# Kernel tuning notes

Hardware: AMD Instinct MI355X
Metric: run time of the kernel (lower is better)

The kernel has to match this reference:

```python
import jax, jax.numpy as jnp
import numpy as np

B, L, H = 16, 2048, 768
V, D = 30000, 64


def setup_inputs() -> dict:
    key = jax.random.key(0)
    k1, k2, k3, k4 = jax.random.split(key, 4)
    bert_x = jax.random.normal(k1, (B, L, H), dtype=jnp.float32)
    x = jax.random.randint(k2, (B, L), 0, V, dtype=jnp.int64)
    ae = jax.random.normal(k3, (V, D), dtype=jnp.float32)
    w = jax.random.normal(k4, (D, D), dtype=jnp.float32)
    return {"bert_x": bert_x, "x": x, "ae": ae, "w": w}


def reference(bert_x, x, ae, w):
    # E[b,i] = ae[x[b,i]]  -> [B, L, D]
    E = ae[x]
    # fac[b,i,j] = E[b,i] @ w @ E[b,j]   (bilinear pairwise score)
    scores = jnp.einsum('bid,de,bje->bij', E, w, E)
    Lseq = bert_x.shape[1]
    i = jnp.arange(Lseq, dtype=bert_x.dtype)[:, None]
    j = jnp.arange(Lseq, dtype=bert_x.dtype)[None, :]
    # strictly-causal weight (i+1)/(j+1) for i < j, zero elsewhere
    coef = jnp.where(i < j, (i + 1.0) / (j + 1.0), 0.0).astype(bert_x.dtype)
    # res[:, j] = bert_x[:, j] + sum_{i<j} bert_x[:, i] * coef[i,j] * fac[b,i,j]
    res = bert_x + jnp.einsum('bij,bih->bjh', scores * coef, bert_x)
    return res
```

## Files before the change

kernel.cpp:

```cpp
#include <hip/hip_runtime.h>

#define Bb 16
#define Ll 2048
#define Hh 768
#define Dd 64
#define Cc 64
#define HC 48
#define NT (Hh / HC)
#define NCH (Ll / Cc)

typedef __attribute__((ext_vector_type(8))) short bf16x8;
typedef __attribute__((ext_vector_type(4))) float f32x4;

__device__ __forceinline__ short f2bf(float f) {
  union { float f; unsigned u; } c;
  c.f = f;
  unsigned r = (c.u + 0x7FFFu + ((c.u >> 16) & 1u)) >> 16;
  return (short)r;
}
__device__ __forceinline__ unsigned pack2(float a, float b) {
  return (unsigned)(unsigned short)f2bf(a) | ((unsigned)(unsigned short)f2bf(b) << 16);
}

__global__ __launch_bounds__(256) void prep_kernel(const int* __restrict__ x,
                                                   const float* __restrict__ ae,
                                                   const float* __restrict__ w,
                                                   short* __restrict__ Eg,
                                                   short* __restrict__ FTg,
                                                   short* __restrict__ scTg) {
  const int b = blockIdx.x >> 5;
  const int ch = blockIdx.x & 31;
  const int tid = threadIdx.x;
  __shared__ float sE[64 * 68];
  __shared__ float sW[64 * 68];
  __shared__ float sF[64 * 68];
  const size_t gb = (size_t)blockIdx.x * 4096;

  {
    const int i = tid >> 2, seg = tid & 3;
    const int idx = x[b * Ll + ch * Cc + i];
    const float4* aer = (const float4*)(ae + (size_t)idx * Dd);
    float4 ev[4];
#pragma unroll
    for (int q = 0; q < 4; ++q) {
      ev[q] = aer[seg * 4 + q];
      *(float4*)&sE[i * 68 + seg * 16 + q * 4] = ev[q];
    }
    uint4 p0v, p1v;
    p0v.x = pack2(ev[0].x, ev[0].y); p0v.y = pack2(ev[0].z, ev[0].w);
    p0v.z = pack2(ev[1].x, ev[1].y); p0v.w = pack2(ev[1].z, ev[1].w);
    p1v.x = pack2(ev[2].x, ev[2].y); p1v.y = pack2(ev[2].z, ev[2].w);
    p1v.z = pack2(ev[3].x, ev[3].y); p1v.w = pack2(ev[3].z, ev[3].w);
    *(uint4*)(Eg + gb + i * 64 + seg * 16) = p0v;
    *(uint4*)(Eg + gb + i * 64 + seg * 16 + 8) = p1v;
    const float4* wr = (const float4*)w;
#pragma unroll
    for (int q = 0; q < 4; ++q) {
      const int fl = q * 256 + tid;
      const int r = fl >> 4, cc = fl & 15;
      *(float4*)&sW[r * 68 + cc * 4] = wr[fl];
    }
  }
  __syncthreads();

  {
    const int i0 = (tid >> 4) * 4, e0 = (tid & 15) * 4;
    float accF[4][4] = {};
    for (int d = 0; d < 64; ++d) {
      float e4[4];
#pragma unroll
      for (int a = 0; a < 4; ++a) e4[a] = sE[(i0 + a) * 68 + d];
      const float4 wv = *(const float4*)&sW[d * 68 + e0];
#pragma unroll
      for (int a = 0; a < 4; ++a) {
        accF[a][0] = fmaf(e4[a], wv.x, accF[a][0]);
        accF[a][1] = fmaf(e4[a], wv.y, accF[a][1]);
        accF[a][2] = fmaf(e4[a], wv.z, accF[a][2]);
        accF[a][3] = fmaf(e4[a], wv.w, accF[a][3]);
      }
    }
#pragma unroll
    for (int a = 0; a < 4; ++a) *(float4*)&sF[(i0 + a) * 68 + e0] = *(float4*)accF[a];
  }
  __syncthreads();

  {
    const int d = tid >> 2, iseg = tid & 3;
    float t[16];
#pragma unroll
    for (int q = 0; q < 16; ++q) t[q] = sF[(iseg * 16 + q) * 68 + d];
    uint4 a0, a1;
    a0.x = pack2(t[0], t[1]);  a0.y = pack2(t[2], t[3]);
    a0.z = pack2(t[4], t[5]);  a0.w = pack2(t[6], t[7]);
    a1.x = pack2(t[8], t[9]);  a1.y = pack2(t[10], t[11]);
    a1.z = pack2(t[12], t[13]); a1.w = pack2(t[14], t[15]);
    *(uint4*)(FTg + gb + d * 64 + iseg * 16) = a0;
    *(uint4*)(FTg + gb + d * 64 + iseg * 16 + 8) = a1;
  }

  {
    const int j0 = (tid >> 4) * 4, i0 = (tid & 15) * 4;
    float acc[4][4] = {};
    for (int d4 = 0; d4 < 16; ++d4) {
      float4 fv[4], ev[4];
#pragma unroll
      for (int q = 0; q < 4; ++q) {
        fv[q] = *(const float4*)&sF[(i0 + q) * 68 + d4 * 4];
        ev[q] = *(const float4*)&sE[(j0 + q) * 68 + d4 * 4];
      }
#pragma unroll
      for (int a = 0; a < 4; ++a)
#pragma unroll
        for (int q = 0; q < 4; ++q)
          acc[a][q] += ev[a].x * fv[q].x + ev[a].y * fv[q].y +
                       ev[a].z * fv[q].z + ev[a].w * fv[q].w;
    }
#pragma unroll
    for (int a = 0; a < 4; ++a) {
      const int j = j0 + a;
      float m[4];
#pragma unroll
      for (int q = 0; q < 4; ++q) m[q] = (i0 + q < j) ? acc[a][q] : 0.f;
      uint2 pv;
      pv.x = pack2(m[0], m[1]);
      pv.y = pack2(m[2], m[3]);
      *(uint2*)(scTg + gb + j * 64 + i0) = pv;
    }
  }
}

__global__ __launch_bounds__(256) void scan_kernel(const float* __restrict__ bx,
                                                   const short* __restrict__ Eg,
                                                   const short* __restrict__ FTg,
                                                   const short* __restrict__ scTg,
                                                   float* __restrict__ out) {
  const int tile = blockIdx.x;
  const int b = blockIdx.y;
  const int tid = threadIdx.x;
  const int w = tid >> 6;
  const int lane = tid & 63;
  const int quad = lane >> 4;
  const int lq = lane & 15;

  __shared__ short sE[64 * 64];
  __shared__ short sSc[64 * 64];
  __shared__ short sFT[64 * 64];
  __shared__ short sGT[48 * 64];
  __shared__ short sST[48 * 64];

  for (int k2 = tid; k2 < 48 * 64 / 2; k2 += 256) ((int*)sST)[k2] = 0;
  f32x4 accS[3] = {};
  __syncthreads();

  for (int ch = 0; ch < NCH; ++ch) {
    const int p0 = ch * Cc;
    const size_t tb = (size_t)(b * NCH + ch) * 4096;

    {
      const uint4* gE = (const uint4*)(Eg + tb);
      const uint4* gS = (const uint4*)(scTg + tb);
      const uint4* gF = (const uint4*)(FTg + tb);
#pragma unroll
      for (int t2 = 0; t2 < 2; ++t2) {
        const int idx = t2 * 256 + tid;
        const int r = idx >> 3, bl = idx & 7;
        const int dst = r * 64 + ((bl ^ (r & 7)) << 3);
        *(uint4*)&sE[dst] = gE[idx];
        *(uint4*)&sSc[dst] = gS[idx];
        *(uint4*)&sFT[dst] = gF[idx];
      }
      const int i = tid >> 2, hs = tid & 3;
      const float* xr = bx + ((size_t)(b * Ll) + p0 + i) * Hh + tile * HC;
      const float scal = (float)(p0 + i + 1);
#pragma unroll
      for (int k = 0; k < 3; ++k) {
        float4 v = *(const float4*)(xr + hs * 4 + k * 16);
        float vv[4] = {v.x, v.y, v.z, v.w};
#pragma unroll
        for (int c = 0; c < 4; ++c) {
          const int h = hs * 4 + k * 16 + c;
          sGT[h * 64 + (((i >> 3) ^ (h & 7)) << 3) + (i & 7)] = f2bf(vv[c] * scal);
        }
      }
    }
    __syncthreads();

    f32x4 accO[3] = {};
    {
      const int rj = w * 16 + lq;
      bf16x8 aC1[2], aC2[2], bD[2];
#pragma unroll
      for (int ks = 0; ks < 2; ++ks) {
        const int blk = ((ks * 4 + quad) ^ (rj & 7)) << 3;
        aC1[ks] = *(const bf16x8*)(sSc + rj * 64 + blk);
        aC2[ks] = *(const bf16x8*)(sE + rj * 64 + blk);
        bD[ks] = *(const bf16x8*)(sFT + rj * 64 + blk);
      }
#pragma unroll
      for (int ht = 0; ht < 3; ++ht) {
        const int rh = ht * 16 + lq;
#pragma unroll
        for (int ks = 0; ks < 2; ++ks) {
          const int blk = ((ks * 4 + quad) ^ (rh & 7)) << 3;
          bf16x8 g = *(const bf16x8*)(sGT + rh * 64 + blk);
          bf16x8 st = *(const bf16x8*)(sST + rh * 64 + blk);
          accO[ht] = __builtin_amdgcn_mfma_f32_16x16x32_bf16(aC1[ks], g, accO[ht], 0, 0, 0);
          accO[ht] = __builtin_amdgcn_mfma_f32_16x16x32_bf16(aC2[ks], st, accO[ht], 0, 0, 0);
          accS[ht] = __builtin_amdgcn_mfma_f32_16x16x32_bf16(g, bD[ks], accS[ht], 0, 0, 0);
        }
      }
    }

#pragma unroll
    for (int ht = 0; ht < 3; ++ht) {
#pragma unroll
      for (int r = 0; r < 4; ++r) {
        const int j = w * 16 + quad * 4 + r;
        const int gj = p0 + j;
        const size_t off = ((size_t)(b * Ll) + gj) * Hh + tile * HC + ht * 16 + lq;
        out[off] = bx[off] + accO[ht][r] * (1.0f / (float)(gj + 1));
      }
    }
    __syncthreads();

#pragma unroll
    for (int ht = 0; ht < 3; ++ht) {
#pragma unroll
      for (int r = 0; r < 4; ++r) {
        const int h = ht * 16 + quad * 4 + r;
        const int d = w * 16 + lq;
        sST[h * 64 + (((d >> 3) ^ (h & 7)) << 3) + (d & 7)] = f2bf(accS[ht][r]);
      }
    }
  }
}

extern "C" void kernel_launch(void* const* d_in, const int* in_sizes, int n_in,
                              void* d_out, int out_size, void* d_ws, size_t ws_size,
                              hipStream_t stream) {
  (void)in_sizes; (void)n_in; (void)out_size; (void)ws_size;
  const float* bx = (const float*)d_in[0];
  const int* x = (const int*)d_in[1];
  const float* ae = (const float*)d_in[2];
  const float* w = (const float*)d_in[3];
  float* out = (float*)d_out;
  short* Eg = (short*)d_ws;
  short* FTg = Eg + (size_t)512 * 4096;
  short* scTg = FTg + (size_t)512 * 4096;

  prep_kernel<<<Bb * NCH, 256, 0, stream>>>(x, ae, w, Eg, FTg, scTg);
  dim3 grid(NT, Bb);
  scan_kernel<<<grid, 256, 0, stream>>>(bx, Eg, FTg, scTg, out);
}
```

Measured before the change: 313.9 us.

## Prefetch next chunk into registers in scan and use MFMA in prep kernel

The scan kernel now loads the next chunk's E/score/FT tiles, bert_x slices and residual values into registers while the current chunk computes, and writes them to LDS after a barrier. This hides global latency behind the MFMA work. The sST state write moves before the compute, and a custom waitcnt+barrier replaces __syncthreads. The prep kernel replaces its scalar fp32 FMA matmuls with bf16 MFMA, which reduces prep precision and raises register pressure in scan.

```diff
diff --git a/kernel.cpp b/kernel.cpp
--- a/kernel.cpp
+++ b/kernel.cpp
@@ -22,109 +22,104 @@
   return (unsigned)(unsigned short)f2bf(a) | ((unsigned)(unsigned short)f2bf(b) << 16);
 }
 
+__device__ __forceinline__ void sync_lds() {
+  asm volatile("s_waitcnt lgkmcnt(0)\n\ts_barrier" ::: "memory");
+}
+
 __global__ __launch_bounds__(256) void prep_kernel(const int* __restrict__ x,
                                                    const float* __restrict__ ae,
                                                    const float* __restrict__ w,
                                                    short* __restrict__ Eg,
                                                    short* __restrict__ FTg,
                                                    short* __restrict__ scTg) {
-  const int b = blockIdx.x >> 5;
-  const int ch = blockIdx.x & 31;
   const int tid = threadIdx.x;
-  __shared__ float sE[64 * 68];
-  __shared__ float sW[64 * 68];
-  __shared__ float sF[64 * 68];
+  const int wv = tid >> 6, lane = tid & 63, quad = lane >> 4, lq = lane & 15;
+  const int b = blockIdx.x >> 5, ch = blockIdx.x & 31;
   const size_t gb = (size_t)blockIdx.x * 4096;
+  __shared__ short sE[64 * 64];
+  __shared__ short sWT[64 * 64];
+  __shared__ short sF[64 * 64];
 
   {
     const int i = tid >> 2, seg = tid & 3;
     const int idx = x[b * Ll + ch * Cc + i];
-    const float4* aer = (const float4*)(ae + (size_t)idx * Dd);
+    const float4* aer = (const float4*)(ae + (size_t)idx * Dd) + seg * 4;
     float4 ev[4];
 #pragma unroll
-    for (int q = 0; q < 4; ++q) {
-      ev[q] = aer[seg * 4 + q];
-      *(float4*)&sE[i * 68 + seg * 16 + q * 4] = ev[q];
-    }
-    uint4 p0v, p1v;
-    p0v.x = pack2(ev[0].x, ev[0].y); p0v.y = pack2(ev[0].z, ev[0].w);
-    p0v.z = pack2(ev[1].x, ev[1].y); p0v.w = pack2(ev[1].z, ev[1].w);
-    p1v.x = pack2(ev[2].x, ev[2].y); p1v.y = pack2(ev[2].z, ev[2].w);
-    p1v.z = pack2(ev[3].x, ev[3].y); p1v.w = pack2(ev[3].z, ev[3].w);
-    *(uint4*)(Eg + gb + i * 64 + seg * 16) = p0v;
-    *(uint4*)(Eg + gb + i * 64 + seg * 16 + 8) = p1v;
+    for (int q = 0; q < 4; ++q) ev[q] = aer[q];
+    uint4 pA, pB;
+    pA.x = pack2(ev[0].x, ev[0].y); pA.y = pack2(ev[0].z, ev[0].w);
+    pA.z = pack2(ev[1].x, ev[1].y); pA.w = pack2(ev[1].z, ev[1].w);
+    pB.x = pack2(ev[2].x, ev[2].y); pB.y = pack2(ev[2].z, ev[2].w);
+    pB.z = pack2(ev[3].x, ev[3].y); pB.w = pack2(ev[3].z, ev[3].w);
+    *(uint4*)&sE[i * 64 + (((2 * seg) ^ (i & 7)) << 3)] = pA;
+    *(uint4*)&sE[i * 64 + (((2 * seg + 1) ^ (i & 7)) << 3)] = pB;
+    *(uint4*)(Eg + gb + i * 64 + seg * 16) = pA;
+    *(uint4*)(Eg + gb + i * 64 + seg * 16 + 8) = pB;
     const float4* wr = (const float4*)w;
 #pragma unroll
     for (int q = 0; q < 4; ++q) {
       const int fl = q * 256 + tid;
-      const int r = fl >> 4, cc = fl & 15;
-      *(float4*)&sW[r * 68 + cc * 4] = wr[fl];
+      const int d = fl >> 4, es = (fl & 15) * 4;
+      const float4 v = wr[fl];
+      const float vv[4] = {v.x, v.y, v.z, v.w};
+#pragma unroll
+      for (int c = 0; c < 4; ++c) {
+        const int e = es + c;
+        sWT[e * 64 + (((d >> 3) ^ (e & 7)) << 3) + (d & 7)] = f2bf(vv[c]);
+      }
     }
   }
   __syncthreads();
 
-  {
-    const int i0 = (tid >> 4) * 4, e0 = (tid & 15) * 4;
-    float accF[4][4] = {};
-    for (int d = 0; d < 64; ++d) {
-      float e4[4];
-#pragma unroll
-      for (int a = 0; a < 4; ++a) e4[a] = sE[(i0 + a) * 68 + d];
-      const float4 wv = *(const float4*)&sW[d * 68 + e0];
-#pragma unroll
-      for (int a = 0; a < 4; ++a) {
-        accF[a][0] = fmaf(e4[a], wv.x, accF[a][0]);
-        accF[a][1] = fmaf(e4[a], wv.y, accF[a][1]);
-        accF[a][2] = fmaf(e4[a], wv.z, accF[a][2]);
-        accF[a][3] = fmaf(e4[a], wv.w, accF[a][3]);
-      }
-    }
-#pragma unroll
-    for (int a = 0; a < 4; ++a) *(float4*)&sF[(i0 + a) * 68 + e0] = *(float4*)accF[a];
+  const int rm = wv * 16 + lq;
+  bf16x8 aE[2], aW[2];
+#pragma unroll
+  for (int ks = 0; ks < 2; ++ks) {
+    const int blk = ((ks * 4 + quad) ^ (rm & 7)) << 3;
+    aE[ks] = *(const bf16x8*)&sE[rm * 64 + blk];
+    aW[ks] = *(const bf16x8*)&sWT[rm * 64 + blk];
+  }
+
+#pragma unroll
+  for (int nt = 0; nt < 4; ++nt) {
+    const int rn = nt * 16 + lq;
+    f32x4 accF = {}, accT = {};
+#pragma unroll
+    for (int ks = 0; ks < 2; ++ks) {
+      const int blk = ((ks * 4 + quad) ^ (rn & 7)) << 3;
+      const bf16x8 bW = *(const bf16x8*)&sWT[rn * 64 + blk];
+      const bf16x8 bE = *(const bf16x8*)&sE[rn * 64 + blk];
+      accF = __builtin_amdgcn_mfma_f32_16x16x32_bf16(aE[ks], bW, accF, 0, 0, 0);
+      accT = __builtin_amdgcn_mfma_f32_16x16x32_bf16(aW[ks], bE, accT, 0, 0, 0);
+    }
+#pragma unroll
+    for (int r = 0; r < 4; ++r) {
+      const int i = wv * 16 + quad * 4 + r;
+      const int e = nt * 16 + lq;
+      sF[i * 64 + (((e >> 3) ^ (i & 7)) << 3) + (e & 7)] = f2bf(accF[r]);
+      const int e2 = wv * 16 + quad * 4 + r;
+      const int i2 = nt * 16 + lq;
+      FTg[gb + e2 * 64 + i2] = f2bf(accT[r]);
+    }
   }
   __syncthreads();
 
-  {
-    const int d = tid >> 2, iseg = tid & 3;
-    float t[16];
-#pragma unroll
-    for (int q = 0; q < 16; ++q) t[q] = sF[(iseg * 16 + q) * 68 + d];
-    uint4 a0, a1;
-    a0.x = pack2(t[0], t[1]);  a0.y = pack2(t[2], t[3]);
-    a0.z = pack2(t[4], t[5]);  a0.w = pack2(t[6], t[7]);
-    a1.x = pack2(t[8], t[9]);  a1.y = pack2(t[10], t[11]);
-    a1.z = pack2(t[12], t[13]); a1.w = pack2(t[14], t[15]);
-    *(uint4*)(FTg + gb + d * 64 + iseg * 16) = a0;
-    *(uint4*)(FTg + gb + d * 64 + iseg * 16 + 8) = a1;
-  }
-
-  {
-    const int j0 = (tid >> 4) * 4, i0 = (tid & 15) * 4;
-    float acc[4][4] = {};
-    for (int d4 = 0; d4 < 16; ++d4) {
-      float4 fv[4], ev[4];
-#pragma unroll
-      for (int q = 0; q < 4; ++q) {
-        fv[q] = *(const float4*)&sF[(i0 + q) * 68 + d4 * 4];
-        ev[q] = *(const float4*)&sE[(j0 + q) * 68 + d4 * 4];
-      }
-#pragma unroll
-      for (int a = 0; a < 4; ++a)
-#pragma unroll
-        for (int q = 0; q < 4; ++q)
-          acc[a][q] += ev[a].x * fv[q].x + ev[a].y * fv[q].y +
-                       ev[a].z * fv[q].z + ev[a].w * fv[q].w;
-    }
-#pragma unroll
-    for (int a = 0; a < 4; ++a) {
-      const int j = j0 + a;
-      float m[4];
-#pragma unroll
-      for (int q = 0; q < 4; ++q) m[q] = (i0 + q < j) ? acc[a][q] : 0.f;
-      uint2 pv;
-      pv.x = pack2(m[0], m[1]);
-      pv.y = pack2(m[2], m[3]);
-      *(uint2*)(scTg + gb + j * 64 + i0) = pv;
+#pragma unroll
+  for (int nt = 0; nt < 4; ++nt) {
+    const int rn = nt * 16 + lq;
+    f32x4 acc = {};
+#pragma unroll
+    for (int ks = 0; ks < 2; ++ks) {
+      const int blk = ((ks * 4 + quad) ^ (rn & 7)) << 3;
+      const bf16x8 bF = *(const bf16x8*)&sF[rn * 64 + blk];
+      acc = __builtin_amdgcn_mfma_f32_16x16x32_bf16(aE[ks], bF, acc, 0, 0, 0);
+    }
+#pragma unroll
+    for (int r = 0; r < 4; ++r) {
+      const int j = wv * 16 + quad * 4 + r;
+      const int i = nt * 16 + lq;
+      scTg[gb + j * 64 + i] = f2bf(i < j ? acc[r] : 0.f);
     }
   }
 }
@@ -137,10 +132,7 @@
   const int tile = blockIdx.x;
   const int b = blockIdx.y;
   const int tid = threadIdx.x;
-  const int w = tid >> 6;
-  const int lane = tid & 63;
-  const int quad = lane >> 4;
-  const int lq = lane & 15;
+  const int w = tid >> 6, lane = tid & 63, quad = lane >> 4, lq = lane & 15;
 
   __shared__ short sE[64 * 64];
   __shared__ short sSc[64 * 64];
@@ -148,42 +140,83 @@
   __shared__ short sGT[48 * 64];
   __shared__ short sST[48 * 64];
 
-  for (int k2 = tid; k2 < 48 * 64 / 2; k2 += 256) ((int*)sST)[k2] = 0;
   f32x4 accS[3] = {};
-  __syncthreads();
+  uint4 rE[2], rS[2], rF[2];
+  float2 rG[6];
+  float rB[12];
+
+  const int ip = tid & 31, hg = tid >> 5;
+
+  auto load_chunk = [&](int ch) {
+    const size_t tb = (size_t)(b * NCH + ch) * 4096;
+    const uint4* gE = (const uint4*)(Eg + tb);
+    const uint4* gS = (const uint4*)(scTg + tb);
+    const uint4* gF = (const uint4*)(FTg + tb);
+#pragma unroll
+    for (int t2 = 0; t2 < 2; ++t2) {
+      const int idx = t2 * 256 + tid;
+      rE[t2] = gE[idx];
+      rS[t2] = gS[idx];
+      rF[t2] = gF[idx];
+    }
+    const int p0 = ch * Cc;
+    const float* xr = bx + ((size_t)(b * Ll) + p0 + 2 * ip) * Hh + tile * HC + hg * 6;
+#pragma unroll
+    for (int k = 0; k < 3; ++k) {
+      rG[k] = *(const float2*)(xr + 2 * k);
+      rG[3 + k] = *(const float2*)(xr + Hh + 2 * k);
+    }
+    const float* br = bx + ((size_t)(b * Ll) + p0 + w * 16 + quad * 4) * Hh + tile * HC + lq;
+#pragma unroll
+    for (int ht = 0; ht < 3; ++ht)
+#pragma unroll
+      for (int r = 0; r < 4; ++r) rB[ht * 4 + r] = br[(size_t)r * Hh + ht * 16];
+  };
+
+  load_chunk(0);
 
   for (int ch = 0; ch < NCH; ++ch) {
     const int p0 = ch * Cc;
-    const size_t tb = (size_t)(b * NCH + ch) * 4096;
-
+    sync_lds();
+
+#pragma unroll
+    for (int t2 = 0; t2 < 2; ++t2) {
+      const int idx = t2 * 256 + tid;
+      const int r_ = idx >> 3, bl = idx & 7;
+      const int dst = r_ * 64 + ((bl ^ (r_ & 7)) << 3);
+      *(uint4*)&sE[dst] = rE[t2];
+      *(uint4*)&sSc[dst] = rS[t2];
+      *(uint4*)&sFT[dst] = rF[t2];
+    }
     {
-      const uint4* gE = (const uint4*)(Eg + tb);
-      const uint4* gS = (const uint4*)(scTg + tb);
-      const uint4* gF = (const uint4*)(FTg + tb);
-#pragma unroll
-      for (int t2 = 0; t2 < 2; ++t2) {
-        const int idx = t2 * 256 + tid;
-        const int r = idx >> 3, bl = idx & 7;
-        const int dst = r * 64 + ((bl ^ (r & 7)) << 3);
-        *(uint4*)&sE[dst] = gE[idx];
-        *(uint4*)&sSc[dst] = gS[idx];
-        *(uint4*)&sFT[dst] = gF[idx];
-      }
-      const int i = tid >> 2, hs = tid & 3;
-      const float* xr = bx + ((size_t)(b * Ll) + p0 + i) * Hh + tile * HC;
-      const float scal = (float)(p0 + i + 1);
+      const float s0 = (float)(p0 + 2 * ip + 1), s1 = (float)(p0 + 2 * ip + 2);
 #pragma unroll
       for (int k = 0; k < 3; ++k) {
-        float4 v = *(const float4*)(xr + hs * 4 + k * 16);
-        float vv[4] = {v.x, v.y, v.z, v.w};
-#pragma unroll
-        for (int c = 0; c < 4; ++c) {
-          const int h = hs * 4 + k * 16 + c;
-          sGT[h * 64 + (((i >> 3) ^ (h & 7)) << 3) + (i & 7)] = f2bf(vv[c] * scal);
+#pragma unroll
+        for (int c = 0; c < 2; ++c) {
+          const int h = hg * 6 + 2 * k + c;
+          const float g0 = (c ? rG[k].y : rG[k].x) * s0;
+          const float g1 = (c ? rG[3 + k].y : rG[3 + k].x) * s1;
+          const int sa = h * 64 + (((ip >> 2) ^ (h & 7)) << 3) + 2 * (ip & 3);
+          *(unsigned*)&sGT[sa] = pack2(g0, g1);
         }
       }
     }
-    __syncthreads();
+#pragma unroll
+    for (int ht = 0; ht < 3; ++ht)
+#pragma unroll
+      for (int r = 0; r < 4; ++r) {
+        const int h = ht * 16 + quad * 4 + r;
+        const int d = w * 16 + lq;
+        sST[h * 64 + (((d >> 3) ^ (h & 7)) << 3) + (d & 7)] = f2bf(accS[ht][r]);
+      }
+
+    float myB[12];
+#pragma unroll
+    for (int q = 0; q < 12; ++q) myB[q] = rB[q];
+    load_chunk(ch + 1 < NCH ? ch + 1 : NCH - 1);
+
+    sync_lds();
 
     f32x4 accO[3] = {};
     {
@@ -215,21 +248,9 @@
     for (int ht = 0; ht < 3; ++ht) {
 #pragma unroll
       for (int r = 0; r < 4; ++r) {
-        const int j = w * 16 + quad * 4 + r;
-        const int gj = p0 + j;
+        const int gj = p0 + w * 16 + quad * 4 + r;
         const size_t off = ((size_t)(b * Ll) + gj) * Hh + tile * HC + ht * 16 + lq;
-        out[off] = bx[off] + accO[ht][r] * (1.0f / (float)(gj + 1));
-      }
-    }
-    __syncthreads();
-
-#pragma unroll
-    for (int ht = 0; ht < 3; ++ht) {
-#pragma unroll
-      for (int r = 0; r < 4; ++r) {
-        const int h = ht * 16 + quad * 4 + r;
-        const int d = w * 16 + lq;
-        sST[h * 64 + (((d >> 3) ^ (h & 7)) << 3) + (d & 7)] = f2bf(accS[ht][r]);
+        out[off] = myB[ht * 4 + r] + accO[ht][r] * (1.0f / (float)(gj + 1));
       }
     }
   }
```

Measured after the change: 254.5 us. 1.23x faster.
